# Optimization experiments

Hardware: AMD Instinct MI355X
Metric: run time of the kernel (lower is better)

## Reference

```python
import jax, jax.numpy as jnp
import numpy as np

NUM_EXPERTS = 4
TOPK = 1
TEMPERATURE = 1.0
NORM_TOPK_PROB = True
N_CLS = 1
N_REL = 4


def setup_inputs() -> dict:
    key = jax.random.key(0)
    ks = jax.random.split(key, 7)
    B, N_total, D, r, E = 64, 1029, 768, 64, NUM_EXPERTS
    x = jax.random.normal(ks[0], (B, N_total, D), dtype=jnp.float32)
    # parameters (torch Linear convention: weight [out, in])
    Wd = jax.random.normal(ks[1], (r, D), dtype=jnp.float32) * (1.0 / np.sqrt(D))
    Wg = jax.random.normal(ks[2], (E, r), dtype=jnp.float32) * (1.0 / np.sqrt(r))
    We = jax.random.normal(ks[3], (E, r, r), dtype=jnp.float32) * (1.0 / np.sqrt(r))
    be = jax.random.normal(ks[4], (E, r), dtype=jnp.float32) * 0.01
    Wu = jax.random.normal(ks[5], (D, r), dtype=jnp.float32) * (1.0 / np.sqrt(r))
    gamma = jnp.ones((D,), dtype=jnp.float32)  # LayerScale init_values=1.0
    return {"x": x, "Wd": Wd, "Wg": Wg, "We": We, "be": be, "Wu": Wu, "gamma": gamma}


def reference(x, Wd, Wg, We, be, Wu, gamma):
    # proj_down (bias=False) + exact GELU (nn.GELU default)
    h = jax.nn.gelu(jnp.einsum('bnd,rd->bnr', x, Wd), approximate=False)  # [B,Nt,r]
    cls_tok = h[:, :N_CLS, :]
    rel_tok = h[:, N_CLS:N_CLS + N_REL, :]
    t = h[:, N_CLS + N_REL:, :]                                           # [B,N,r]
    B, N, r = t.shape

    # gating: softmax scores, top-k selection
    logits = jnp.einsum('bnr,er->bne', t, Wg) / TEMPERATURE
    scores = jax.nn.softmax(logits, axis=-1)                              # [B,N,E]
    topk_w, topk_idx = jax.lax.top_k(scores, TOPK)                        # [B,N,K]
    if TOPK > 1 and NORM_TOPK_PROB:
        topk_w = topk_w / jnp.sum(topk_w, axis=-1, keepdims=True)

    # experts are tiny Linear(r,r): compute all experts densely, then gather.
    # Same math as per-expert gather/GEMM/scatter-combine in the source.
    expert_all = jnp.einsum('bnr,esr->bnes', t, We) + be                  # [B,N,E,r]
    idx_b = jnp.broadcast_to(topk_idx[..., None], (B, N, TOPK, r))
    sel = jnp.take_along_axis(expert_all, idx_b, axis=2)                  # [B,N,K,r]
    combine = jnp.sum(sel * topk_w[..., None], axis=2)                    # [B,N,r]

    full = jnp.concatenate([cls_tok, rel_tok, t + combine], axis=1)       # [B,Nt,r]
    # proj_up (bias=False) + LayerScale
    return jnp.einsum('bnr,dr->bnd', full, Wu) * gamma
```

## Files before the change

kernel.cpp:

```cpp
#include <hip/hip_runtime.h>
#include <math.h>


#define GELU(v) (0.5f*(v)*(1.0f + erff((v)*0.70710678118654752440f)))

typedef __attribute__((ext_vector_type(8))) short bf16x8;
typedef __attribute__((ext_vector_type(4))) float f32x4;

#define MFMA(a,b,c) __builtin_amdgcn_mfma_f32_16x16x32_bf16((a),(b),(c),0,0,0)

__device__ __forceinline__ unsigned pk_hi(float a, float b) {
  return (__float_as_uint(a) >> 16) | (__float_as_uint(b) & 0xFFFF0000u);
}
__device__ __forceinline__ float f_lo(float a) {
  return a - __uint_as_float(__float_as_uint(a) & 0xFFFF0000u);
}
__device__ __forceinline__ int swz(int row, int kbyte) {
  return row*128 + (kbyte ^ ((row & 7) << 4));
}
__device__ __forceinline__ void split_store(char* hiB, char* loB, int row, int kg,
                                            float4 f0, float4 f1) {
  uint4 hv, lv;
  hv.x = pk_hi(f0.x, f0.y); hv.y = pk_hi(f0.z, f0.w);
  hv.z = pk_hi(f1.x, f1.y); hv.w = pk_hi(f1.z, f1.w);
  lv.x = pk_hi(f_lo(f0.x), f_lo(f0.y)); lv.y = pk_hi(f_lo(f0.z), f_lo(f0.w));
  lv.z = pk_hi(f_lo(f1.x), f_lo(f1.y)); lv.w = pk_hi(f_lo(f1.z), f_lo(f1.w));
  int off = swz(row, kg << 4);
  *(uint4*)(hiB + off) = hv;
  *(uint4*)(loB + off) = lv;
}
__device__ __forceinline__ bf16x8 frag_ld(const char* b, int row, int kbyte) {
  return *(const bf16x8*)(b + swz(row, kbyte));
}

__global__ __launch_bounds__(256) void k1_proj_gelu(
    const float* __restrict__ x, const float* __restrict__ Wd,
    float* __restrict__ h)
{
  __shared__ uint4 AhS[512], AlS[512], BhS[512], BlS[512];
  char* Ah = (char*)AhS; char* Al = (char*)AlS;
  char* Bh = (char*)BhS; char* Bl = (char*)BlS;
  const int tid = threadIdx.x;
  const int bm  = blockIdx.x;
  const int wv = tid >> 6, l = tid & 63;
  const int lg = l >> 4, lr = l & 15;
  const float* xblk = x + (size_t)bm * (64*768);

  f32x4 acc[4];
  #pragma unroll
  for (int i = 0; i < 4; ++i)
    #pragma unroll
    for (int j = 0; j < 4; ++j) acc[i][j] = 0.f;

  for (int kt = 0; kt < 768; kt += 64) {
    #pragma unroll
    for (int it = 0; it < 2; ++it) {
      int li = it*256 + tid;
      int row = li >> 3, kg = li & 7;
      const float* p = xblk + row*768 + kt + kg*8;
      float4 f0 = *(const float4*)p, f1 = *(const float4*)(p+4);
      split_store(Ah, Al, row, kg, f0, f1);
      const float* q = Wd + row*768 + kt + kg*8;
      float4 g0 = *(const float4*)q, g1 = *(const float4*)(q+4);
      split_store(Bh, Bl, row, kg, g0, g1);
    }
    __syncthreads();
    #pragma unroll
    for (int kc = 0; kc < 2; ++kc) {
      int kb = kc*64 + lg*16;
      bf16x8 ah = frag_ld(Ah, wv*16 + lr, kb);
      bf16x8 al = frag_ld(Al, wv*16 + lr, kb);
      #pragma unroll
      for (int nt = 0; nt < 4; ++nt) {
        bf16x8 bh = frag_ld(Bh, nt*16 + lr, kb);
        bf16x8 bl = frag_ld(Bl, nt*16 + lr, kb);
        acc[nt] = MFMA(ah, bh, acc[nt]);
        acc[nt] = MFMA(ah, bl, acc[nt]);
        acc[nt] = MFMA(al, bh, acc[nt]);
      }
    }
    __syncthreads();
  }
  #pragma unroll
  for (int nt = 0; nt < 4; ++nt)
    #pragma unroll
    for (int r = 0; r < 4; ++r) {
      int token = bm*64 + wv*16 + lg*4 + r;
      float v = acc[nt][r];
      h[(size_t)token*64 + nt*16 + lr] = GELU(v);
    }
}

__global__ __launch_bounds__(256) void k2_moe(
    const float* __restrict__ Wg, const float* __restrict__ We,
    const float* __restrict__ be, float* __restrict__ h)
{
  __shared__ uint4 AhS[512], AlS[512];
  __shared__ uint4 BhS[2176], BlS[2176];
  __shared__ float sBe[256];
  char* Ah = (char*)AhS; char* Al = (char*)AlS;
  char* Bh = (char*)BhS; char* Bl = (char*)BlS;
  const int tid = threadIdx.x;
  const int bm  = blockIdx.x;
  const int wv = tid >> 6, l = tid & 63;
  const int lg = l >> 4, lr = l & 15;

  for (int i = tid; i < 2176; i += 256) {
    int col = i >> 3, kg = i & 7;
    float4 f0, f1;
    if (col < 256) {
      const float* p = We + (size_t)col*64 + kg*8;
      f0 = *(const float4*)p; f1 = *(const float4*)(p+4);
    } else if (col < 260) {
      const float* p = Wg + (col-256)*64 + kg*8;
      f0 = *(const float4*)p; f1 = *(const float4*)(p+4);
    } else {
      f0 = make_float4(0.f,0.f,0.f,0.f); f1 = f0;
    }
    split_store(Bh, Bl, col, kg, f0, f1);
  }
  sBe[tid] = be[tid];
  #pragma unroll
  for (int it = 0; it < 2; ++it) {
    int li = it*256 + tid;
    int row = li >> 3, kg = li & 7;
    int mt = bm*64 + row;
    int token = (mt >> 10)*1029 + 5 + (mt & 1023);
    const float* p = h + (size_t)token*64 + kg*8;
    float4 f0 = *(const float4*)p, f1 = *(const float4*)(p+4);
    split_store(Ah, Al, row, kg, f0, f1);
  }
  __syncthreads();

  f32x4 acc[17];
  #pragma unroll
  for (int i = 0; i < 17; ++i)
    #pragma unroll
    for (int j = 0; j < 4; ++j) acc[i][j] = 0.f;

  #pragma unroll
  for (int kc = 0; kc < 2; ++kc) {
    int kb = kc*64 + lg*16;
    bf16x8 ah = frag_ld(Ah, wv*16 + lr, kb);
    bf16x8 al = frag_ld(Al, wv*16 + lr, kb);
    #pragma unroll
    for (int nt = 0; nt < 17; ++nt) {
      bf16x8 bh = frag_ld(Bh, nt*16 + lr, kb);
      bf16x8 bl = frag_ld(Bl, nt*16 + lr, kb);
      acc[nt] = MFMA(ah, bh, acc[nt]);
      acc[nt] = MFMA(ah, bl, acc[nt]);
      acc[nt] = MFMA(al, bh, acc[nt]);
    }
  }

  #pragma unroll
  for (int r = 0; r < 4; ++r) {
    float lt = acc[16][r];
    int base = l & 48;
    float l0 = __shfl(lt, base + 0);
    float l1 = __shfl(lt, base + 1);
    float l2 = __shfl(lt, base + 2);
    float l3 = __shfl(lt, base + 3);
    int ei = 0; float lm = l0;
    if (l1 > lm) { lm = l1; ei = 1; }
    if (l2 > lm) { lm = l2; ei = 2; }
    if (l3 > lm) { lm = l3; ei = 3; }
    float s = expf(l0-lm)+expf(l1-lm)+expf(l2-lm)+expf(l3-lm);
    float w = 1.0f / s;
    int mt = bm*64 + wv*16 + lg*4 + r;
    size_t tbase = (size_t)((mt >> 10)*1029 + 5 + (mt & 1023))*64;
    #pragma unroll
    for (int j = 0; j < 4; ++j) {
      float d0 = acc[j][r], d1 = acc[4+j][r], d2 = acc[8+j][r], d3 = acc[12+j][r];
      float dsel = d0;
      dsel = (ei == 1) ? d1 : dsel;
      dsel = (ei == 2) ? d2 : dsel;
      dsel = (ei == 3) ? d3 : dsel;
      int col = j*16 + lr;
      float bev = sBe[ei*64 + col];
      float tv = h[tbase + col];
      h[tbase + col] = tv + w * (dsel + bev);
    }
  }
}

__global__ __launch_bounds__(256) void k3_up_gamma(
    const float* __restrict__ h, const float* __restrict__ Wu,
    const float* __restrict__ gamma, float* __restrict__ out)
{
  __shared__ uint4 AhS[512], AlS[512];
  __shared__ uint4 BhS[1024], BlS[1024];
  char* Ah = (char*)AhS; char* Al = (char*)AlS;
  char* Bh = (char*)BhS; char* Bl = (char*)BlS;
  const int tid = threadIdx.x;
  const int bm  = blockIdx.x;
  const int wv = tid >> 6, l = tid & 63;
  const int lg = l >> 4, lr = l & 15;

  #pragma unroll
  for (int it = 0; it < 2; ++it) {
    int li = it*256 + tid;
    int row = li >> 3, kg = li & 7;
    const float* p = h + (size_t)(bm*64 + row)*64 + kg*8;
    float4 f0 = *(const float4*)p, f1 = *(const float4*)(p+4);
    split_store(Ah, Al, row, kg, f0, f1);
  }

  for (int c = 0; c < 6; ++c) {
    if (c) __syncthreads();
    #pragma unroll
    for (int it = 0; it < 4; ++it) {
      int li = it*256 + tid;
      int row = li >> 3, kg = li & 7;
      const float* p = Wu + (size_t)(c*128 + row)*64 + kg*8;
      float4 f0 = *(const float4*)p, f1 = *(const float4*)(p+4);
      split_store(Bh, Bl, row, kg, f0, f1);
    }
    __syncthreads();

    f32x4 acc[8];
    #pragma unroll
    for (int i = 0; i < 8; ++i)
      #pragma unroll
      for (int j = 0; j < 4; ++j) acc[i][j] = 0.f;

    #pragma unroll
    for (int kc = 0; kc < 2; ++kc) {
      int kb = kc*64 + lg*16;
      bf16x8 ah = frag_ld(Ah, wv*16 + lr, kb);
      bf16x8 al = frag_ld(Al, wv*16 + lr, kb);
      #pragma unroll
      for (int nt = 0; nt < 8; ++nt) {
        bf16x8 bh = frag_ld(Bh, nt*16 + lr, kb);
        bf16x8 bl = frag_ld(Bl, nt*16 + lr, kb);
        acc[nt] = MFMA(ah, bh, acc[nt]);
        acc[nt] = MFMA(ah, bl, acc[nt]);
        acc[nt] = MFMA(al, bh, acc[nt]);
      }
    }
    #pragma unroll
    for (int nt = 0; nt < 8; ++nt) {
      int col = c*128 + nt*16 + lr;
      float gv = gamma[col];
      #pragma unroll
      for (int r = 0; r < 4; ++r) {
        int token = bm*64 + wv*16 + lg*4 + r;
        out[(size_t)token*768 + col] = acc[nt][r] * gv;
      }
    }
  }
}

extern "C" void kernel_launch(void* const* d_in, const int* in_sizes, int n_in,
                              void* d_out, int out_size, void* d_ws, size_t ws_size,
                              hipStream_t stream) {
  const float* x     = (const float*)d_in[0];
  const float* Wd    = (const float*)d_in[1];
  const float* Wg    = (const float*)d_in[2];
  const float* We    = (const float*)d_in[3];
  const float* be    = (const float*)d_in[4];
  const float* Wu    = (const float*)d_in[5];
  const float* gamma = (const float*)d_in[6];
  float* out = (float*)d_out;
  float* h   = (float*)d_ws;

  k1_proj_gelu<<<1029, 256, 0, stream>>>(x, Wd, h);
  k2_moe<<<1024, 256, 0, stream>>>(Wg, We, be, h);
  k3_up_gamma<<<1029, 256, 0, stream>>>(h, Wu, gamma, out);
}
```

Baseline: 438.8 us.

## Fuse down-proj, MoE and up-proj into one kernel with prepacked bf16 weights

Replaces the three-kernel pipeline with a small weight-prepacking kernel plus one fused kernel. Each wave computes proj-down+GELU, the gate and expert matmuls, and proj-up for its 16 tokens, passing intermediates through a per-wave shared-memory tile. This removes the h round-trip through global memory and two launches. Weights are pre-split into hi/lo bf16 fragments in MFMA-ready order and read straight from global/L2, so the kernel drops the LDS staging and block-wide barriers. In exchange each block reads the x rows uncoalesced per lane, computes all four experts per token, and relies on L2 hits for the repeated weight loads.

```diff
diff --git a/kernel.cpp b/kernel.cpp
--- a/kernel.cpp
+++ b/kernel.cpp
@@ -15,239 +15,216 @@
 __device__ __forceinline__ float f_lo(float a) {
   return a - __uint_as_float(__float_as_uint(a) & 0xFFFF0000u);
 }
-__device__ __forceinline__ int swz(int row, int kbyte) {
-  return row*128 + (kbyte ^ ((row & 7) << 4));
-}
-__device__ __forceinline__ void split_store(char* hiB, char* loB, int row, int kg,
-                                            float4 f0, float4 f1) {
-  uint4 hv, lv;
-  hv.x = pk_hi(f0.x, f0.y); hv.y = pk_hi(f0.z, f0.w);
-  hv.z = pk_hi(f1.x, f1.y); hv.w = pk_hi(f1.z, f1.w);
-  lv.x = pk_hi(f_lo(f0.x), f_lo(f0.y)); lv.y = pk_hi(f_lo(f0.z), f_lo(f0.w));
-  lv.z = pk_hi(f_lo(f1.x), f_lo(f1.y)); lv.w = pk_hi(f_lo(f1.z), f_lo(f1.w));
-  int off = swz(row, kg << 4);
-  *(uint4*)(hiB + off) = hv;
-  *(uint4*)(loB + off) = lv;
-}
-__device__ __forceinline__ bf16x8 frag_ld(const char* b, int row, int kbyte) {
-  return *(const bf16x8*)(b + swz(row, kbyte));
-}
-
-__global__ __launch_bounds__(256) void k1_proj_gelu(
-    const float* __restrict__ x, const float* __restrict__ Wd,
-    float* __restrict__ h)
+union U8 { unsigned u[4]; bf16x8 v; uint4 q; };
+__device__ __forceinline__ bf16x8 hi8(float4 f0, float4 f1) {
+  U8 r; r.u[0]=pk_hi(f0.x,f0.y); r.u[1]=pk_hi(f0.z,f0.w);
+        r.u[2]=pk_hi(f1.x,f1.y); r.u[3]=pk_hi(f1.z,f1.w); return r.v;
+}
+__device__ __forceinline__ bf16x8 lo8(float4 f0, float4 f1) {
+  U8 r; r.u[0]=pk_hi(f_lo(f0.x),f_lo(f0.y)); r.u[1]=pk_hi(f_lo(f0.z),f_lo(f0.w));
+        r.u[2]=pk_hi(f_lo(f1.x),f_lo(f1.y)); r.u[3]=pk_hi(f_lo(f1.z),f_lo(f1.w)); return r.v;
+}
+
+__global__ __launch_bounds__(256) void prep_pack(
+    const float* __restrict__ Wd, const float* __restrict__ Wg,
+    const float* __restrict__ We, const float* __restrict__ Wu,
+    char* __restrict__ wp)
 {
-  __shared__ uint4 AhS[512], AlS[512], BhS[512], BlS[512];
-  char* Ah = (char*)AhS; char* Al = (char*)AlS;
-  char* Bh = (char*)BhS; char* Bl = (char*)BlS;
-  const int tid = threadIdx.x;
-  const int bm  = blockIdx.x;
-  const int wv = tid >> 6, l = tid & 63;
-  const int lg = l >> 4, lr = l & 15;
-  const float* xblk = x + (size_t)bm * (64*768);
-
-  f32x4 acc[4];
-  #pragma unroll
-  for (int i = 0; i < 4; ++i)
-    #pragma unroll
-    for (int j = 0; j < 4; ++j) acc[i][j] = 0.f;
-
-  for (int kt = 0; kt < 768; kt += 64) {
-    #pragma unroll
-    for (int it = 0; it < 2; ++it) {
-      int li = it*256 + tid;
-      int row = li >> 3, kg = li & 7;
-      const float* p = xblk + row*768 + kt + kg*8;
-      float4 f0 = *(const float4*)p, f1 = *(const float4*)(p+4);
-      split_store(Ah, Al, row, kg, f0, f1);
-      const float* q = Wd + row*768 + kt + kg*8;
-      float4 g0 = *(const float4*)q, g1 = *(const float4*)(q+4);
-      split_store(Bh, Bl, row, kg, g0, g1);
-    }
-    __syncthreads();
+  int fid = blockIdx.x*4 + (threadIdx.x >> 6);
+  if (fid >= 452) return;
+  int lane = threadIdx.x & 63, lg = lane >> 4, lr = lane & 15;
+  float v[8];
+  int part;
+  if (fid < 192) {
+    part = fid & 1; int q = fid >> 1;
+    int nt = q & 3; q >>= 2; int kc = q & 1, kt = q >> 1;
+    int col = nt*16 + lr, k = kt*64 + kc*32 + lg*8;
+    const float* p = Wd + (size_t)col*768 + k;
+    #pragma unroll
+    for (int e = 0; e < 8; ++e) v[e] = p[e];
+  } else if (fid < 260) {
+    int f = fid - 192; part = f & 1; int q = f >> 1;
+    int nt = q % 17, kc = q / 17;
+    int col = nt*16 + lr, k = kc*32 + lg*8;
+    if (col < 256) {
+      const float* p = We + (size_t)col*64 + k;
+      #pragma unroll
+      for (int e = 0; e < 8; ++e) v[e] = p[e];
+    } else if (col < 260) {
+      const float* p = Wg + (size_t)(col-256)*64 + k;
+      #pragma unroll
+      for (int e = 0; e < 8; ++e) v[e] = p[e];
+    } else {
+      #pragma unroll
+      for (int e = 0; e < 8; ++e) v[e] = 0.f;
+    }
+  } else {
+    int f = fid - 260; part = f & 1; int q = f >> 1;
+    int kc = q & 1, nt = q >> 1;
+    int col = nt*16 + lr, k = kc*32 + lg*8;
+    const float* p = Wu + (size_t)col*64 + k;
+    #pragma unroll
+    for (int e = 0; e < 8; ++e) v[e] = p[e];
+  }
+  U8 r;
+  if (part == 0) {
+    r.u[0]=pk_hi(v[0],v[1]); r.u[1]=pk_hi(v[2],v[3]);
+    r.u[2]=pk_hi(v[4],v[5]); r.u[3]=pk_hi(v[6],v[7]);
+  } else {
+    r.u[0]=pk_hi(f_lo(v[0]),f_lo(v[1])); r.u[1]=pk_hi(f_lo(v[2]),f_lo(v[3]));
+    r.u[2]=pk_hi(f_lo(v[4]),f_lo(v[5])); r.u[3]=pk_hi(f_lo(v[6]),f_lo(v[7]));
+  }
+  *(uint4*)(wp + (size_t)fid*1024 + lane*16) = r.q;
+}
+
+__global__ __launch_bounds__(256) void fused(
+    const float* __restrict__ x, const float* __restrict__ be,
+    const float* __restrict__ gamma, const char* __restrict__ wp,
+    float* __restrict__ out)
+{
+  __shared__ float sF[4][16][68];
+  const int tid = threadIdx.x, bm = blockIdx.x;
+  const int wv = tid >> 6, l = tid & 63, lg = l >> 4, lr = l & 15;
+  const char* wpL = wp + l*16;
+
+  const float* xrow = x + (size_t)(bm*64 + wv*16 + lr)*768;
+  f32x4 t4[4];
+  #pragma unroll
+  for (int nt = 0; nt < 4; ++nt)
+    #pragma unroll
+    for (int r = 0; r < 4; ++r) t4[nt][r] = 0.f;
+
+  for (int kt = 0; kt < 12; ++kt) {
     #pragma unroll
     for (int kc = 0; kc < 2; ++kc) {
-      int kb = kc*64 + lg*16;
-      bf16x8 ah = frag_ld(Ah, wv*16 + lr, kb);
-      bf16x8 al = frag_ld(Al, wv*16 + lr, kb);
+      const float* xp = xrow + kt*64 + kc*32 + lg*8;
+      float4 f0 = *(const float4*)xp, f1 = *(const float4*)(xp + 4);
+      bf16x8 ah = hi8(f0, f1), al = lo8(f0, f1);
+      const char* bp = wpL + (size_t)((kt*2 + kc)*8)*1024;
       #pragma unroll
       for (int nt = 0; nt < 4; ++nt) {
-        bf16x8 bh = frag_ld(Bh, nt*16 + lr, kb);
-        bf16x8 bl = frag_ld(Bl, nt*16 + lr, kb);
-        acc[nt] = MFMA(ah, bh, acc[nt]);
-        acc[nt] = MFMA(ah, bl, acc[nt]);
-        acc[nt] = MFMA(al, bh, acc[nt]);
+        bf16x8 bh = *(const bf16x8*)(bp + (nt*2+0)*1024);
+        bf16x8 bl = *(const bf16x8*)(bp + (nt*2+1)*1024);
+        t4[nt] = MFMA(ah, bh, t4[nt]);
+        t4[nt] = MFMA(ah, bl, t4[nt]);
+        t4[nt] = MFMA(al, bh, t4[nt]);
       }
     }
-    __syncthreads();
   }
   #pragma unroll
   for (int nt = 0; nt < 4; ++nt)
     #pragma unroll
     for (int r = 0; r < 4; ++r) {
-      int token = bm*64 + wv*16 + lg*4 + r;
-      float v = acc[nt][r];
-      h[(size_t)token*64 + nt*16 + lr] = GELU(v);
-    }
-}
-
-__global__ __launch_bounds__(256) void k2_moe(
-    const float* __restrict__ Wg, const float* __restrict__ We,
-    const float* __restrict__ be, float* __restrict__ h)
-{
-  __shared__ uint4 AhS[512], AlS[512];
-  __shared__ uint4 BhS[2176], BlS[2176];
-  __shared__ float sBe[256];
-  char* Ah = (char*)AhS; char* Al = (char*)AlS;
-  char* Bh = (char*)BhS; char* Bl = (char*)BlS;
-  const int tid = threadIdx.x;
-  const int bm  = blockIdx.x;
-  const int wv = tid >> 6, l = tid & 63;
-  const int lg = l >> 4, lr = l & 15;
-
-  for (int i = tid; i < 2176; i += 256) {
-    int col = i >> 3, kg = i & 7;
-    float4 f0, f1;
-    if (col < 256) {
-      const float* p = We + (size_t)col*64 + kg*8;
-      f0 = *(const float4*)p; f1 = *(const float4*)(p+4);
-    } else if (col < 260) {
-      const float* p = Wg + (col-256)*64 + kg*8;
-      f0 = *(const float4*)p; f1 = *(const float4*)(p+4);
-    } else {
-      f0 = make_float4(0.f,0.f,0.f,0.f); f1 = f0;
-    }
-    split_store(Bh, Bl, col, kg, f0, f1);
-  }
-  sBe[tid] = be[tid];
-  #pragma unroll
-  for (int it = 0; it < 2; ++it) {
-    int li = it*256 + tid;
-    int row = li >> 3, kg = li & 7;
-    int mt = bm*64 + row;
-    int token = (mt >> 10)*1029 + 5 + (mt & 1023);
-    const float* p = h + (size_t)token*64 + kg*8;
-    float4 f0 = *(const float4*)p, f1 = *(const float4*)(p+4);
-    split_store(Ah, Al, row, kg, f0, f1);
-  }
-  __syncthreads();
-
-  f32x4 acc[17];
-  #pragma unroll
-  for (int i = 0; i < 17; ++i)
-    #pragma unroll
-    for (int j = 0; j < 4; ++j) acc[i][j] = 0.f;
-
+      float g = GELU(t4[nt][r]);
+      t4[nt][r] = g;
+      sF[wv][lg*4 + r][nt*16 + lr] = g;
+    }
+
+  bf16x8 pah[2], pal[2];
   #pragma unroll
   for (int kc = 0; kc < 2; ++kc) {
-    int kb = kc*64 + lg*16;
-    bf16x8 ah = frag_ld(Ah, wv*16 + lr, kb);
-    bf16x8 al = frag_ld(Al, wv*16 + lr, kb);
-    #pragma unroll
-    for (int nt = 0; nt < 17; ++nt) {
-      bf16x8 bh = frag_ld(Bh, nt*16 + lr, kb);
-      bf16x8 bl = frag_ld(Bl, nt*16 + lr, kb);
-      acc[nt] = MFMA(ah, bh, acc[nt]);
-      acc[nt] = MFMA(ah, bl, acc[nt]);
-      acc[nt] = MFMA(al, bh, acc[nt]);
-    }
-  }
-
+    const float* ap = &sF[wv][lr][kc*32 + lg*8];
+    float4 a0 = *(const float4*)ap, a1 = *(const float4*)(ap + 4);
+    pah[kc] = hi8(a0, a1); pal[kc] = lo8(a0, a1);
+  }
+  f32x4 lac;
+  #pragma unroll
+  for (int r = 0; r < 4; ++r) lac[r] = 0.f;
+  #pragma unroll
+  for (int kc = 0; kc < 2; ++kc) {
+    const char* bp = wpL + (size_t)(192 + (kc*17 + 16)*2)*1024;
+    bf16x8 bh = *(const bf16x8*)(bp);
+    bf16x8 bl = *(const bf16x8*)(bp + 1024);
+    lac = MFMA(pah[kc], bh, lac);
+    lac = MFMA(pah[kc], bl, lac);
+    lac = MFMA(pal[kc], bh, lac);
+  }
+  const int tokbase = bm*64 + wv*16 + lg*4;
+  float w_[4]; int ei_[4];
   #pragma unroll
   for (int r = 0; r < 4; ++r) {
-    float lt = acc[16][r];
+    float lt = lac[r];
     int base = l & 48;
-    float l0 = __shfl(lt, base + 0);
-    float l1 = __shfl(lt, base + 1);
-    float l2 = __shfl(lt, base + 2);
-    float l3 = __shfl(lt, base + 3);
+    float l0 = __shfl(lt, base+0), l1 = __shfl(lt, base+1);
+    float l2 = __shfl(lt, base+2), l3 = __shfl(lt, base+3);
     int ei = 0; float lm = l0;
     if (l1 > lm) { lm = l1; ei = 1; }
     if (l2 > lm) { lm = l2; ei = 2; }
     if (l3 > lm) { lm = l3; ei = 3; }
-    float s = expf(l0-lm)+expf(l1-lm)+expf(l2-lm)+expf(l3-lm);
+    float s = expf(l0-lm) + expf(l1-lm) + expf(l2-lm) + expf(l3-lm);
     float w = 1.0f / s;
-    int mt = bm*64 + wv*16 + lg*4 + r;
-    size_t tbase = (size_t)((mt >> 10)*1029 + 5 + (mt & 1023))*64;
+    int pos = (tokbase + r) % 1029;
+    if (pos < 5) w = 0.0f;
+    w_[r] = w; ei_[r] = ei;
+  }
+  f32x4 sel[4];
+  #pragma unroll
+  for (int j = 0; j < 4; ++j)
+    #pragma unroll
+    for (int r = 0; r < 4; ++r) sel[j][r] = 0.f;
+  #pragma unroll
+  for (int e = 0; e < 4; ++e) {
+    f32x4 de[4];
+    #pragma unroll
+    for (int j = 0; j < 4; ++j)
+      #pragma unroll
+      for (int r = 0; r < 4; ++r) de[j][r] = 0.f;
+    #pragma unroll
+    for (int kc = 0; kc < 2; ++kc) {
+      const char* bp = wpL + (size_t)(192 + (kc*17 + e*4)*2)*1024;
+      #pragma unroll
+      for (int j = 0; j < 4; ++j) {
+        bf16x8 bh = *(const bf16x8*)(bp + (j*2+0)*1024);
+        bf16x8 bl = *(const bf16x8*)(bp + (j*2+1)*1024);
+        de[j] = MFMA(pah[kc], bh, de[j]);
+        de[j] = MFMA(pah[kc], bl, de[j]);
+        de[j] = MFMA(pal[kc], bh, de[j]);
+      }
+    }
+    #pragma unroll
+    for (int j = 0; j < 4; ++j)
+      #pragma unroll
+      for (int r = 0; r < 4; ++r)
+        sel[j][r] = (ei_[r] == e) ? de[j][r] : sel[j][r];
+  }
+  #pragma unroll
+  for (int r = 0; r < 4; ++r) {
     #pragma unroll
     for (int j = 0; j < 4; ++j) {
-      float d0 = acc[j][r], d1 = acc[4+j][r], d2 = acc[8+j][r], d3 = acc[12+j][r];
-      float dsel = d0;
-      dsel = (ei == 1) ? d1 : dsel;
-      dsel = (ei == 2) ? d2 : dsel;
-      dsel = (ei == 3) ? d3 : dsel;
       int col = j*16 + lr;
-      float bev = sBe[ei*64 + col];
-      float tv = h[tbase + col];
-      h[tbase + col] = tv + w * (dsel + bev);
-    }
-  }
-}
-
-__global__ __launch_bounds__(256) void k3_up_gamma(
-    const float* __restrict__ h, const float* __restrict__ Wu,
-    const float* __restrict__ gamma, float* __restrict__ out)
-{
-  __shared__ uint4 AhS[512], AlS[512];
-  __shared__ uint4 BhS[1024], BlS[1024];
-  char* Ah = (char*)AhS; char* Al = (char*)AlS;
-  char* Bh = (char*)BhS; char* Bl = (char*)BlS;
-  const int tid = threadIdx.x;
-  const int bm  = blockIdx.x;
-  const int wv = tid >> 6, l = tid & 63;
-  const int lg = l >> 4, lr = l & 15;
-
-  #pragma unroll
-  for (int it = 0; it < 2; ++it) {
-    int li = it*256 + tid;
-    int row = li >> 3, kg = li & 7;
-    const float* p = h + (size_t)(bm*64 + row)*64 + kg*8;
-    float4 f0 = *(const float4*)p, f1 = *(const float4*)(p+4);
-    split_store(Ah, Al, row, kg, f0, f1);
-  }
-
-  for (int c = 0; c < 6; ++c) {
-    if (c) __syncthreads();
-    #pragma unroll
-    for (int it = 0; it < 4; ++it) {
-      int li = it*256 + tid;
-      int row = li >> 3, kg = li & 7;
-      const float* p = Wu + (size_t)(c*128 + row)*64 + kg*8;
-      float4 f0 = *(const float4*)p, f1 = *(const float4*)(p+4);
-      split_store(Bh, Bl, row, kg, f0, f1);
-    }
-    __syncthreads();
-
-    f32x4 acc[8];
-    #pragma unroll
-    for (int i = 0; i < 8; ++i)
-      #pragma unroll
-      for (int j = 0; j < 4; ++j) acc[i][j] = 0.f;
-
-    #pragma unroll
-    for (int kc = 0; kc < 2; ++kc) {
-      int kb = kc*64 + lg*16;
-      bf16x8 ah = frag_ld(Ah, wv*16 + lr, kb);
-      bf16x8 al = frag_ld(Al, wv*16 + lr, kb);
-      #pragma unroll
-      for (int nt = 0; nt < 8; ++nt) {
-        bf16x8 bh = frag_ld(Bh, nt*16 + lr, kb);
-        bf16x8 bl = frag_ld(Bl, nt*16 + lr, kb);
-        acc[nt] = MFMA(ah, bh, acc[nt]);
-        acc[nt] = MFMA(ah, bl, acc[nt]);
-        acc[nt] = MFMA(al, bh, acc[nt]);
-      }
-    }
-    #pragma unroll
-    for (int nt = 0; nt < 8; ++nt) {
-      int col = c*128 + nt*16 + lr;
-      float gv = gamma[col];
-      #pragma unroll
-      for (int r = 0; r < 4; ++r) {
-        int token = bm*64 + wv*16 + lg*4 + r;
-        out[(size_t)token*768 + col] = acc[nt][r] * gv;
-      }
-    }
+      float full = t4[j][r] + w_[r] * (sel[j][r] + be[ei_[r]*64 + col]);
+      sF[wv][lg*4 + r][col] = full;
+    }
+  }
+
+  bf16x8 a3h[2], a3l[2];
+  #pragma unroll
+  for (int kc = 0; kc < 2; ++kc) {
+    const float* ap = &sF[wv][lr][kc*32 + lg*8];
+    float4 a0 = *(const float4*)ap, a1 = *(const float4*)(ap + 4);
+    a3h[kc] = hi8(a0, a1); a3l[kc] = lo8(a0, a1);
+  }
+  #pragma unroll 4
+  for (int nt = 0; nt < 48; ++nt) {
+    const char* bp = wpL + (size_t)(260 + nt*4)*1024;
+    f32x4 o;
+    #pragma unroll
+    for (int r = 0; r < 4; ++r) o[r] = 0.f;
+    bf16x8 b0h = *(const bf16x8*)(bp);
+    bf16x8 b0l = *(const bf16x8*)(bp + 1024);
+    bf16x8 b1h = *(const bf16x8*)(bp + 2048);
+    bf16x8 b1l = *(const bf16x8*)(bp + 3072);
+    o = MFMA(a3h[0], b0h, o);
+    o = MFMA(a3h[0], b0l, o);
+    o = MFMA(a3l[0], b0h, o);
+    o = MFMA(a3h[1], b1h, o);
+    o = MFMA(a3h[1], b1l, o);
+    o = MFMA(a3l[1], b1h, o);
+    int col = nt*16 + lr;
+    float g = gamma[col];
+    #pragma unroll
+    for (int r = 0; r < 4; ++r)
+      out[(size_t)(tokbase + r)*768 + col] = o[r] * g;
   }
 }
 
@@ -262,9 +239,8 @@
   const float* Wu    = (const float*)d_in[5];
   const float* gamma = (const float*)d_in[6];
   float* out = (float*)d_out;
-  float* h   = (float*)d_ws;
-
-  k1_proj_gelu<<<1029, 256, 0, stream>>>(x, Wd, h);
-  k2_moe<<<1024, 256, 0, stream>>>(Wg, We, be, h);
-  k3_up_gamma<<<1029, 256, 0, stream>>>(h, Wu, gamma, out);
-}
+  char* wp   = (char*)d_ws;
+
+  prep_pack<<<113, 256, 0, stream>>>(Wd, Wg, We, Wu, wp);
+  fused<<<1029, 256, 0, stream>>>(x, be, gamma, (const char*)wp, out);
+}
```

Result: no change. 442.0 us (+0.7%).
